# Optimization experiments

Hardware: AMD Instinct MI355X
Metric: run time of the kernel (lower is better)

## Reference

```python
import jax, jax.numpy as jnp
import numpy as np

N = 50000      # nodes
E = 1600000    # edges (avg degree 32)
F_IN = 128     # num_features
DIM = 64       # hidden dim
L = 3          # num_gc_layers
G = 500        # graphs in batch


def setup_inputs() -> dict:
    key = jax.random.key(0)
    ks = jax.random.split(key, 16)
    inp = {}
    inp["x"] = jax.random.normal(ks[0], (N, F_IN), dtype=jnp.float32)
    inp["edge_index"] = jax.random.randint(ks[1], (2, E), 0, N, dtype=jnp.int32)
    inp["batch"] = jnp.sort(jax.random.randint(ks[2], (N,), 0, G, dtype=jnp.int32))
    # GIN layer MLP params: layer0 maps F_IN->DIM->DIM, later layers DIM->DIM->DIM
    d_in = F_IN
    ki = 3
    for i in range(L):
        inp[f"W1_{i}"] = jax.random.normal(ks[ki], (d_in, DIM), dtype=jnp.float32) / np.sqrt(d_in); ki += 1
        inp[f"b1_{i}"] = jnp.zeros((DIM,), dtype=jnp.float32)
        inp[f"W2_{i}"] = jax.random.normal(ks[ki], (DIM, DIM), dtype=jnp.float32) / np.sqrt(DIM); ki += 1
        inp[f"b2_{i}"] = jnp.zeros((DIM,), dtype=jnp.float32)
        d_in = DIM
    # final scoring head: concat readout -> dim * L inputs, 1 output
    inp["Wm"] = jax.random.normal(ks[ki], (DIM * L, 1), dtype=jnp.float32) / np.sqrt(DIM * L)
    inp["bm"] = jnp.zeros((1,), dtype=jnp.float32)
    return inp


def _segment_softmax(scores, seg, num_segments):
    # numerically stable softmax over elements grouped by seg; scores [M, 1]
    m = jax.ops.segment_max(scores, seg, num_segments=num_segments)
    e = jnp.exp(scores - m[seg])
    denom = jax.ops.segment_sum(e, seg, num_segments=num_segments)
    return e / denom[seg]


def _forward(x, edge_index, batch, params):
    src, dst = edge_index[0], edge_index[1]
    n = x.shape[0]
    xs = []
    h = x
    for i in range(L):
        W1, b1, W2, b2 = params[4 * i: 4 * i + 4]
        # GINConv (eps=0): h_i <- MLP(h_i + sum_{j->i} h_j)
        agg = jax.ops.segment_sum(h[src], dst, num_segments=n)
        h = jax.nn.relu((h + agg) @ W1 + b1) @ W2 + b2
        if i != L - 1:
            h = jax.nn.relu(h)
        xs.append(h)
    node_prob = jnp.concatenate(xs, axis=1)            # concat readout [N, DIM*L]
    Wm, bm = params[4 * L], params[4 * L + 1]
    node_score = node_prob @ Wm + bm                   # [N, 1]
    # lift_node_score_to_edge_score
    src_score = node_score[src]                        # [E, 1]
    dst_score = node_score[dst]
    edge_score = src_score * dst_score
    edge_prop = _segment_softmax(edge_score, dst, n)   # softmax over edges per dst
    new_score = jax.ops.segment_sum(src_score * edge_prop, dst, num_segments=n)
    node_score = node_score + new_score
    # final softmax over nodes grouped by graph id
    return _segment_softmax(node_score, batch, G)


def reference(x, edge_index, batch, W1_0, b1_0, W2_0, b2_0, W1_1, b1_1, W2_1, b2_1,
              W1_2, b1_2, W2_2, b2_2, Wm, bm):
    params = [W1_0, b1_0, W2_0, b2_0, W1_1, b1_1, W2_1, b2_1,
              W1_2, b1_2, W2_2, b2_2, Wm, bm]
    return _forward(x, edge_index, batch, params)
```

## Files before the change

### kernel.cpp

```cpp
#include <hip/hip_runtime.h>
#include <math.h>

#define N_NODES 50000
#define N_EDGES 1600000
#define N_GRAPH 500
#define CHUNKS 64
#define EPC (N_EDGES / CHUNKS)

__device__ __forceinline__ float rl(float v, int k) {
    return __int_as_float(__builtin_amdgcn_readlane(__float_as_int(v), k));
}

__global__ __launch_bounds__(1024) void histsort_kernel(const int* __restrict__ src,
                                                        const int* __restrict__ dst,
                                                        int* __restrict__ csrc_chunk,
                                                        unsigned* __restrict__ cntloc,
                                                        unsigned short* __restrict__ lr_g) {
    __shared__ unsigned packed[N_NODES / 2];
    __shared__ unsigned aux[1024];
    const int c = blockIdx.x;
    const int s0 = c * EPC;
    const int tid = threadIdx.x;

    for (int i = tid; i < N_NODES / 2; i += 1024) packed[i] = 0;
    __syncthreads();

    for (int e = s0 + tid; e < s0 + EPC; e += 1024) {
        int d = dst[e];
        int sh = (d & 1) * 16;
        unsigned old = atomicAdd(&packed[d >> 1], 1u << sh);
        lr_g[e] = (unsigned short)((old >> sh) & 0xffffu);
    }
    __syncthreads();

    const int W = 25;
    int w0 = tid * W;
    int w1 = min(w0 + W, N_NODES / 2);
    unsigned run = 0;
    for (int i = w0; i < w1; i++) {
        unsigned v = packed[i];
        unsigned lo = v & 0xffffu, hi = v >> 16;
        packed[i] = run | ((run + lo) << 16);
        run += lo + hi;
    }
    aux[tid] = run;
    __syncthreads();
    for (int off = 1; off < 1024; off <<= 1) {
        unsigned t = (tid >= off) ? aux[tid - off] : 0;
        __syncthreads();
        aux[tid] += t;
        __syncthreads();
    }
    unsigned b0 = (tid == 0) ? 0 : aux[tid - 1];
    if (b0) {
        unsigned addv = b0 | (b0 << 16);
        for (int i = w0; i < w1; i++) packed[i] += addv;
    }
    __syncthreads();

    int* outc = csrc_chunk + (size_t)c * EPC;
    for (int e = s0 + tid; e < s0 + EPC; e += 1024) {
        int d = dst[e];
        unsigned pw = packed[d >> 1];
        unsigned loc = (d & 1) ? (pw >> 16) : (pw & 0xffffu);
        outc[loc + lr_g[e]] = src[e];
    }
    unsigned* clc = cntloc + (size_t)c * N_NODES;
    for (int d = tid; d < N_NODES; d += 1024) {
        unsigned pw = packed[d >> 1];
        unsigned loc = (d & 1) ? (pw >> 16) : (pw & 0xffffu);
        unsigned nxt;
        if (d + 1 < N_NODES) {
            unsigned pw2 = packed[(d + 1) >> 1];
            nxt = ((d + 1) & 1) ? (pw2 >> 16) : (pw2 & 0xffffu);
        } else {
            nxt = EPC;
        }
        clc[d] = ((nxt - loc) << 16) | loc;
    }
}

__global__ __launch_bounds__(1024) void base_scan1_kernel(const unsigned* __restrict__ cntloc,
                                                          unsigned short* __restrict__ base,
                                                          int* __restrict__ deg,
                                                          int* __restrict__ part, int N) {
    int d = blockIdx.x * 1024 + threadIdx.x;
    int run = 0;
    if (d < N) {
#pragma unroll 8
        for (int c = 0; c < CHUNKS; c++) {
            int v = (int)(cntloc[(size_t)c * N + d] >> 16);
            base[(size_t)c * N + d] = (unsigned short)run;
            run += v;
        }
        deg[d] = run;
    }
    int v = run;
#pragma unroll
    for (int o = 32; o >= 1; o >>= 1) v += __shfl_xor(v, o);
    __shared__ int red[16];
    if ((threadIdx.x & 63) == 0) red[threadIdx.x >> 6] = v;
    __syncthreads();
    if (threadIdx.x == 0) {
        int s = 0;
#pragma unroll
        for (int k = 0; k < 16; k++) s += red[k];
        part[blockIdx.x] = s;
    }
}

__global__ void scan2_kernel(int* __restrict__ part, int nb) {
    int lane = threadIdx.x;
    int v = (lane < nb) ? part[lane] : 0;
    int orig = v;
#pragma unroll
    for (int o = 1; o < 64; o <<= 1) {
        int t = __shfl_up(v, o);
        if (lane >= o) v += t;
    }
    if (lane < nb) part[lane] = v - orig;
    if (lane == nb - 1) part[nb] = v;
}

__global__ __launch_bounds__(1024) void scan3_kernel(const int* __restrict__ deg,
                                                     const int* __restrict__ part,
                                                     int* __restrict__ rowptr, int N) {
    int i = blockIdx.x * 1024 + threadIdx.x;
    int lane = threadIdx.x & 63;
    int w = threadIdx.x >> 6;
    int v = (i < N) ? deg[i] : 0;
    int inc = v;
#pragma unroll
    for (int o = 1; o < 64; o <<= 1) {
        int t = __shfl_up(inc, o);
        if (lane >= o) inc += t;
    }
    __shared__ int wsum[16];
    if (lane == 63) wsum[w] = inc;
    __syncthreads();
    if (threadIdx.x < 16) {
        int x = wsum[threadIdx.x];
        int xo = x;
#pragma unroll
        for (int o = 1; o < 16; o <<= 1) {
            int t = __shfl_up(x, o);
            if ((int)threadIdx.x >= o) x += t;
        }
        wsum[threadIdx.x] = x - xo;
    }
    __syncthreads();
    int b = part[blockIdx.x] + wsum[w];
    if (i < N) {
        rowptr[i] = b + inc - v;
        if (i == N - 1) rowptr[N] = b + inc;
    }
}

__global__ __launch_bounds__(256) void gatherfill_kernel(const int* __restrict__ csrc_chunk,
                                                         const unsigned* __restrict__ cntloc,
                                                         const unsigned short* __restrict__ base,
                                                         const int* __restrict__ rowptr,
                                                         int* __restrict__ csr_src) {
    const int perXcd = N_NODES / 8;
    int xcd = blockIdx.x & 7;
    int idx = (blockIdx.x >> 3) * 4 + ((threadIdx.x) >> 6);
    if (idx >= perXcd) return;
    int wid = xcd * perXcd + idx;
    int lane = threadIdx.x & 63;
    unsigned cl = cntloc[(size_t)lane * N_NODES + wid];
    int cnt = (int)(cl >> 16);
    int loc = (int)(cl & 0xffffu);
    int ob = rowptr[wid] + (int)base[(size_t)lane * N_NODES + wid];
    const int* in = csrc_chunk + (size_t)lane * EPC + loc;
    for (int i = 0; i < cnt; i++) csr_src[ob + i] = in[i];
}

__global__ __launch_bounds__(256) void agg_kernel(const float* __restrict__ y,
                                                  const int* __restrict__ rowptr,
                                                  const int* __restrict__ csr_src,
                                                  float* __restrict__ u, int N) {
    int wid = (blockIdx.x * 256 + threadIdx.x) >> 6;
    int lane = threadIdx.x & 63;
    if (wid >= N) return;
    int q = lane >> 4;
    int r = lane & 15;
    int start = rowptr[wid];
    int end = rowptr[wid + 1];
    float4 acc = make_float4(0.f, 0.f, 0.f, 0.f);
    int j = start;
    for (; j + 32 <= end; j += 32) {
        int s0 = csr_src[j + q];
        int s1 = csr_src[j + 4 + q];
        int s2 = csr_src[j + 8 + q];
        int s3 = csr_src[j + 12 + q];
        int s4 = csr_src[j + 16 + q];
        int s5 = csr_src[j + 20 + q];
        int s6 = csr_src[j + 24 + q];
        int s7 = csr_src[j + 28 + q];
        float4 v0 = *(const float4*)(y + (size_t)s0 * 64 + r * 4);
        float4 v1 = *(const float4*)(y + (size_t)s1 * 64 + r * 4);
        float4 v2 = *(const float4*)(y + (size_t)s2 * 64 + r * 4);
        float4 v3 = *(const float4*)(y + (size_t)s3 * 64 + r * 4);
        float4 v4 = *(const float4*)(y + (size_t)s4 * 64 + r * 4);
        float4 v5 = *(const float4*)(y + (size_t)s5 * 64 + r * 4);
        float4 v6 = *(const float4*)(y + (size_t)s6 * 64 + r * 4);
        float4 v7 = *(const float4*)(y + (size_t)s7 * 64 + r * 4);
        acc.x += ((v0.x + v1.x) + (v2.x + v3.x)) + ((v4.x + v5.x) + (v6.x + v7.x));
        acc.y += ((v0.y + v1.y) + (v2.y + v3.y)) + ((v4.y + v5.y) + (v6.y + v7.y));
        acc.z += ((v0.z + v1.z) + (v2.z + v3.z)) + ((v4.z + v5.z) + (v6.z + v7.z));
        acc.w += ((v0.w + v1.w) + (v2.w + v3.w)) + ((v4.w + v5.w) + (v6.w + v7.w));
    }
#pragma unroll
    for (int m = 0; m < 8; m++) {
        int e = j + 4 * m + q;
        if (e < end) {
            int s = csr_src[e];
            float4 v = *(const float4*)(y + (size_t)s * 64 + r * 4);
            acc.x += v.x; acc.y += v.y; acc.z += v.z; acc.w += v.w;
        }
    }
    acc.x += __shfl_xor(acc.x, 16);
    acc.y += __shfl_xor(acc.y, 16);
    acc.z += __shfl_xor(acc.z, 16);
    acc.w += __shfl_xor(acc.w, 16);
    acc.x += __shfl_xor(acc.x, 32);
    acc.y += __shfl_xor(acc.y, 32);
    acc.z += __shfl_xor(acc.z, 32);
    acc.w += __shfl_xor(acc.w, 32);
    if (lane < 16) {
        float4 self = *(const float4*)(y + (size_t)wid * 64 + r * 4);
        acc.x += self.x; acc.y += self.y; acc.z += self.z; acc.w += self.w;
        *(float4*)(u + (size_t)wid * 64 + r * 4) = acc;
    }
}

__global__ __launch_bounds__(256) void gemm0_kernel(const float* __restrict__ x,
                                                    const float* __restrict__ W1,
                                                    float* __restrict__ y0,
                                                    int N, int totalWaves) {
    int lane = threadIdx.x & 63;
    int wid = (blockIdx.x * 256 + threadIdx.x) >> 6;
    float w[64];
#pragma unroll
    for (int k = 0; k < 64; k++) w[k] = W1[k * 64 + lane];
    for (int node = wid; node < N; node += totalWaves) {
        float xa = x[node * 128 + lane];
        float a0 = 0.f, a1 = 0.f, a2 = 0.f, a3 = 0.f;
#pragma unroll
        for (int k = 0; k < 64; k += 4) {
            a0 = fmaf(rl(xa, k + 0), w[k + 0], a0);
            a1 = fmaf(rl(xa, k + 1), w[k + 1], a1);
            a2 = fmaf(rl(xa, k + 2), w[k + 2], a2);
            a3 = fmaf(rl(xa, k + 3), w[k + 3], a3);
        }
        y0[node * 64 + lane] = (a0 + a1) + (a2 + a3);
    }
#pragma unroll
    for (int k = 0; k < 64; k++) w[k] = W1[(64 + k) * 64 + lane];
    for (int node = wid; node < N; node += totalWaves) {
        float xb = x[node * 128 + 64 + lane];
        float a0 = 0.f, a1 = 0.f, a2 = 0.f, a3 = 0.f;
#pragma unroll
        for (int k = 0; k < 64; k += 4) {
            a0 = fmaf(rl(xb, k + 0), w[k + 0], a0);
            a1 = fmaf(rl(xb, k + 1), w[k + 1], a1);
            a2 = fmaf(rl(xb, k + 2), w[k + 2], a2);
            a3 = fmaf(rl(xb, k + 3), w[k + 3], a3);
        }
        y0[node * 64 + lane] += (a0 + a1) + (a2 + a3);
    }
}

template <int LAYER>
__global__ __launch_bounds__(256) void mlpAB_kernel(const float* __restrict__ u,
                                                    const float* __restrict__ b1,
                                                    const float* __restrict__ W2,
                                                    const float* __restrict__ b2,
                                                    const float* __restrict__ W1n,
                                                    const float* __restrict__ Wm,
                                                    float* __restrict__ ynext,
                                                    float* __restrict__ score,
                                                    int N, int totalWaves) {
    int lane = threadIdx.x & 63;
    int wid = (blockIdx.x * 256 + threadIdx.x) >> 6;
    float w2[64], w1[64];
#pragma unroll
    for (int k = 0; k < 64; k++) w2[k] = W2[k * 64 + lane];
#pragma unroll
    for (int k = 0; k < 64; k++) w1[k] = W1n[k * 64 + lane];
    float bb1 = b1[lane], bb2 = b2[lane], wm = Wm[LAYER * 64 + lane];

    int node = wid;
    float uin = (node < N) ? u[node * 64 + lane] : 0.f;
    for (; node < N; node += totalWaves) {
        int nn = node + totalWaves;
        float unext = (nn < N) ? u[nn * 64 + lane] : 0.f;
        float t = fmaxf(uin + bb1, 0.f);
        float a0 = 0.f, a1 = 0.f, a2 = 0.f, a3 = 0.f;
#pragma unroll
        for (int k = 0; k < 64; k += 4) {
            a0 = fmaf(rl(t, k + 0), w2[k + 0], a0);
            a1 = fmaf(rl(t, k + 1), w2[k + 1], a1);
            a2 = fmaf(rl(t, k + 2), w2[k + 2], a2);
            a3 = fmaf(rl(t, k + 3), w2[k + 3], a3);
        }
        float h = fmaxf(bb2 + ((a0 + a1) + (a2 + a3)), 0.f);
        float p = h * wm;
#pragma unroll
        for (int o = 32; o >= 1; o >>= 1) p += __shfl_xor(p, o);
        if (lane == 0) {
            if (LAYER == 0) score[node] = p;
            else score[node] += p;
        }
        float y0 = 0.f, y1 = 0.f, y2 = 0.f, y3 = 0.f;
#pragma unroll
        for (int k = 0; k < 64; k += 4) {
            y0 = fmaf(rl(h, k + 0), w1[k + 0], y0);
            y1 = fmaf(rl(h, k + 1), w1[k + 1], y1);
            y2 = fmaf(rl(h, k + 2), w1[k + 2], y2);
            y3 = fmaf(rl(h, k + 3), w1[k + 3], y3);
        }
        ynext[node * 64 + lane] = (y0 + y1) + (y2 + y3);
        uin = unext;
    }
}

__global__ __launch_bounds__(256) void mlpA2_kernel(const float* __restrict__ u,
                                                    const float* __restrict__ b1,
                                                    const float* __restrict__ W2,
                                                    const float* __restrict__ b2,
                                                    const float* __restrict__ Wm,
                                                    float* __restrict__ score,
                                                    int N, int totalWaves) {
    int lane = threadIdx.x & 63;
    int wid = (blockIdx.x * 256 + threadIdx.x) >> 6;
    float w2[64];
#pragma unroll
    for (int k = 0; k < 64; k++) w2[k] = W2[k * 64 + lane];
    float bb1 = b1[lane], bb2 = b2[lane], wm = Wm[2 * 64 + lane];

    int node = wid;
    float uin = (node < N) ? u[node * 64 + lane] : 0.f;
    for (; node < N; node += totalWaves) {
        int nn = node + totalWaves;
        float unext = (nn < N) ? u[nn * 64 + lane] : 0.f;
        float t = fmaxf(uin + bb1, 0.f);
        float a0 = 0.f, a1 = 0.f, a2 = 0.f, a3 = 0.f;
#pragma unroll
        for (int k = 0; k < 64; k += 4) {
            a0 = fmaf(rl(t, k + 0), w2[k + 0], a0);
            a1 = fmaf(rl(t, k + 1), w2[k + 1], a1);
            a2 = fmaf(rl(t, k + 2), w2[k + 2], a2);
            a3 = fmaf(rl(t, k + 3), w2[k + 3], a3);
        }
        float h = bb2 + ((a0 + a1) + (a2 + a3));
        float p = h * wm;
#pragma unroll
        for (int o = 32; o >= 1; o >>= 1) p += __shfl_xor(p, o);
        if (lane == 0) score[node] += p;
        uin = unext;
    }
}

__global__ __launch_bounds__(256) void edge_softmax_kernel(const float* __restrict__ score,
                                                           const int* __restrict__ rowptr,
                                                           const int* __restrict__ csr_src,
                                                           const float* __restrict__ bm,
                                                           float* __restrict__ nsf, int N) {
    int wid = (blockIdx.x * blockDim.x + threadIdx.x) >> 6;
    int lane = threadIdx.x & 63;
    if (wid >= N) return;
    float b = bm[0];
    float sd = score[wid] + b;
    int start = rowptr[wid];
    int end = rowptr[wid + 1];
    bool has0 = (start + lane < end);
    float ss0 = 0.f;
    float m = -INFINITY;
    if (has0) {
        ss0 = score[csr_src[start + lane]] + b;
        m = ss0 * sd;
    }
    for (int j = start + 64 + lane; j < end; j += 64) {
        float ss = score[csr_src[j]] + b;
        m = fmaxf(m, ss * sd);
    }
#pragma unroll
    for (int o = 32; o >= 1; o >>= 1) m = fmaxf(m, __shfl_xor(m, o));
    float se = 0.f, swe = 0.f;
    if (m > -INFINITY) {
        if (has0) {
            float e0 = expf(ss0 * sd - m);
            se += e0;
            swe += ss0 * e0;
        }
        for (int j = start + 64 + lane; j < end; j += 64) {
            float ss = score[csr_src[j]] + b;
            float e = expf(ss * sd - m);
            se += e;
            swe += ss * e;
        }
#pragma unroll
        for (int o = 32; o >= 1; o >>= 1) {
            se += __shfl_xor(se, o);
            swe += __shfl_xor(swe, o);
        }
    }
    float ns = (se > 0.f) ? (swe / se) : 0.f;
    if (lane == 0) nsf[wid] = sd + ns;
}

__global__ __launch_bounds__(256) void graph_softmax_kernel(const float* __restrict__ nsf,
                                                            const int* __restrict__ batch,
                                                            float* __restrict__ out, int N) {
    int g = blockIdx.x;
    int tid = threadIdx.x;
    int lo = 0, hi = N;
    while (lo < hi) { int mid = (lo + hi) >> 1; if (batch[mid] < g) lo = mid + 1; else hi = mid; }
    int s0 = lo;
    hi = N;
    while (lo < hi) { int mid = (lo + hi) >> 1; if (batch[mid] < g + 1) lo = mid + 1; else hi = mid; }
    int s1 = lo;

    __shared__ float red[4];
    __shared__ float bval;
    float m = -INFINITY;
    for (int i = s0 + tid; i < s1; i += 256) m = fmaxf(m, nsf[i]);
#pragma unroll
    for (int o = 32; o >= 1; o >>= 1) m = fmaxf(m, __shfl_xor(m, o));
    if ((tid & 63) == 0) red[tid >> 6] = m;
    __syncthreads();
    if (tid == 0) bval = fmaxf(fmaxf(red[0], red[1]), fmaxf(red[2], red[3]));
    __syncthreads();
    float bmx = bval;
    float s = 0.f;
    for (int i = s0 + tid; i < s1; i += 256) {
        float e = expf(nsf[i] - bmx);
        out[i] = e;
        s += e;
    }
#pragma unroll
    for (int o = 32; o >= 1; o >>= 1) s += __shfl_xor(s, o);
    __syncthreads();
    if ((tid & 63) == 0) red[tid >> 6] = s;
    __syncthreads();
    if (tid == 0) bval = red[0] + red[1] + red[2] + red[3];
    __syncthreads();
    float inv = 1.f / bval;
    for (int i = s0 + tid; i < s1; i += 256) out[i] *= inv;
}

extern "C" void kernel_launch(void* const* d_in, const int* in_sizes, int n_in,
                              void* d_out, int out_size, void* d_ws, size_t ws_size,
                              hipStream_t stream) {
    const int N = N_NODES, E = N_EDGES;

    const float* x = (const float*)d_in[0];
    const int* ei = (const int*)d_in[1];
    const int* batch = (const int*)d_in[2];
    const float* W1a[3] = {(const float*)d_in[3], (const float*)d_in[7], (const float*)d_in[11]};
    const float* b1a[3] = {(const float*)d_in[4], (const float*)d_in[8], (const float*)d_in[12]};
    const float* W2a[3] = {(const float*)d_in[5], (const float*)d_in[9], (const float*)d_in[13]};
    const float* b2a[3] = {(const float*)d_in[6], (const float*)d_in[10], (const float*)d_in[14]};
    const float* Wm = (const float*)d_in[15];
    const float* bm = (const float*)d_in[16];
    float* out = (float*)d_out;

    const int* srcp = ei;
    const int* dstp = ei + E;

    float* yA = (float*)d_ws;
    float* yB = yA + (size_t)N * 64;
    float* ubuf = yB + (size_t)N * 64;
    int* csrc_chunk = (int*)ubuf;
    float* score = ubuf + (size_t)N * 64;
    float* nsf = score + N;
    int* deg = (int*)(nsf + N);
    int* rowptr = deg + N;
    int* part = rowptr + N + 1;
    int* csr_src = part + 64;
    unsigned* cntloc = (unsigned*)(csr_src + E);
    unsigned short* base = (unsigned short*)(cntloc + (size_t)CHUNKS * N);
    unsigned short* lr = base + (size_t)CHUNKS * N;

    histsort_kernel<<<CHUNKS, 1024, 0, stream>>>(srcp, dstp, csrc_chunk, cntloc, lr);

    const int nbScan = (N + 1023) / 1024;
    base_scan1_kernel<<<nbScan, 1024, 0, stream>>>(cntloc, base, deg, part, N);
    scan2_kernel<<<1, 64, 0, stream>>>(part, nbScan);
    scan3_kernel<<<nbScan, 1024, 0, stream>>>(deg, part, rowptr, N);

    const int gfBlocks = 8 * ((N / 8 + 3) / 4);
    gatherfill_kernel<<<gfBlocks, 256, 0, stream>>>(csrc_chunk, cntloc, base, rowptr, csr_src);

    const int gw = 4096;
    gemm0_kernel<<<1024, 256, 0, stream>>>(x, W1a[0], yA, N, gw);

    int aggBlocks = (N + 3) / 4;

    agg_kernel<<<aggBlocks, 256, 0, stream>>>(yA, rowptr, csr_src, ubuf, N);
    mlpAB_kernel<0><<<1024, 256, 0, stream>>>(ubuf, b1a[0], W2a[0], b2a[0], W1a[1], Wm, yB, score, N, gw);

    agg_kernel<<<aggBlocks, 256, 0, stream>>>(yB, rowptr, csr_src, ubuf, N);
    mlpAB_kernel<1><<<1024, 256, 0, stream>>>(ubuf, b1a[1], W2a[1], b2a[1], W1a[2], Wm, yA, score, N, gw);

    agg_kernel<<<aggBlocks, 256, 0, stream>>>(yA, rowptr, csr_src, ubuf, N);
    mlpA2_kernel<<<1024, 256, 0, stream>>>(ubuf, b1a[2], W2a[2], b2a[2], Wm, score, N, gw);

    edge_softmax_kernel<<<(N + 3) / 4, 256, 0, stream>>>(score, rowptr, csr_src, bm, nsf, N);

    graph_softmax_kernel<<<N_GRAPH, 256, 0, stream>>>(nsf, batch, out, N);
}
```

Baseline: 374.1 us.

## Double histogram chunks, store compact per-chunk offsets, aggregate two nodes per wave

The CSR build now splits edges into 128 chunks instead of 64 and stores only 16-bit per-chunk start offsets (with a sentinel), deriving counts from adjacent offsets instead of storing packed count/offset words. The gather-fill kernel handles two chunks per lane. The aggregation kernel assigns two consecutive destination nodes to each wave and splits the accumulation by edge index, so short rows waste fewer idle lanes and fewer waves are launched. The trade-offs are per-edge branching in the accumulation, an extra shuffle reduction, and more scan work over the additional chunks.

```diff
diff --git a/kernel.cpp b/kernel.cpp
--- a/kernel.cpp
+++ b/kernel.cpp
@@ -4,8 +4,9 @@
 #define N_NODES 50000
 #define N_EDGES 1600000
 #define N_GRAPH 500
-#define CHUNKS 64
+#define CHUNKS 128
 #define EPC (N_EDGES / CHUNKS)
+#define NP1 (N_NODES + 1)
 
 __device__ __forceinline__ float rl(float v, int k) {
     return __int_as_float(__builtin_amdgcn_readlane(__float_as_int(v), k));
@@ -14,7 +15,7 @@
 __global__ __launch_bounds__(1024) void histsort_kernel(const int* __restrict__ src,
                                                         const int* __restrict__ dst,
                                                         int* __restrict__ csrc_chunk,
-                                                        unsigned* __restrict__ cntloc,
+                                                        unsigned short* __restrict__ locs,
                                                         unsigned short* __restrict__ lr_g) {
     __shared__ unsigned packed[N_NODES / 2];
     __shared__ unsigned aux[1024];
@@ -65,22 +66,20 @@
         unsigned loc = (d & 1) ? (pw >> 16) : (pw & 0xffffu);
         outc[loc + lr_g[e]] = src[e];
     }
-    unsigned* clc = cntloc + (size_t)c * N_NODES;
-    for (int d = tid; d < N_NODES; d += 1024) {
-        unsigned pw = packed[d >> 1];
-        unsigned loc = (d & 1) ? (pw >> 16) : (pw & 0xffffu);
-        unsigned nxt;
-        if (d + 1 < N_NODES) {
-            unsigned pw2 = packed[(d + 1) >> 1];
-            nxt = ((d + 1) & 1) ? (pw2 >> 16) : (pw2 & 0xffffu);
+    unsigned short* lc = locs + (size_t)c * NP1;
+    for (int d = tid; d <= N_NODES; d += 1024) {
+        unsigned short loc;
+        if (d == N_NODES) {
+            loc = (unsigned short)EPC;
         } else {
-            nxt = EPC;
-        }
-        clc[d] = ((nxt - loc) << 16) | loc;
-    }
-}
-
-__global__ __launch_bounds__(1024) void base_scan1_kernel(const unsigned* __restrict__ cntloc,
+            unsigned pw = packed[d >> 1];
+            loc = (unsigned short)((d & 1) ? (pw >> 16) : (pw & 0xffffu));
+        }
+        lc[d] = loc;
+    }
+}
+
+__global__ __launch_bounds__(1024) void base_scan1_kernel(const unsigned short* __restrict__ locs,
                                                           unsigned short* __restrict__ base,
                                                           int* __restrict__ deg,
                                                           int* __restrict__ part, int N) {
@@ -89,9 +88,10 @@
     if (d < N) {
 #pragma unroll 8
         for (int c = 0; c < CHUNKS; c++) {
-            int v = (int)(cntloc[(size_t)c * N + d] >> 16);
+            int l0 = locs[(size_t)c * NP1 + d];
+            int l1 = locs[(size_t)c * NP1 + d + 1];
             base[(size_t)c * N + d] = (unsigned short)run;
-            run += v;
+            run += l1 - l0;
         }
         deg[d] = run;
     }
@@ -157,46 +157,51 @@
 }
 
 __global__ __launch_bounds__(256) void gatherfill_kernel(const int* __restrict__ csrc_chunk,
-                                                         const unsigned* __restrict__ cntloc,
+                                                         const unsigned short* __restrict__ locs,
                                                          const unsigned short* __restrict__ base,
                                                          const int* __restrict__ rowptr,
                                                          int* __restrict__ csr_src) {
     const int perXcd = N_NODES / 8;
     int xcd = blockIdx.x & 7;
-    int idx = (blockIdx.x >> 3) * 4 + ((threadIdx.x) >> 6);
+    int idx = (blockIdx.x >> 3) * 4 + (threadIdx.x >> 6);
     if (idx >= perXcd) return;
     int wid = xcd * perXcd + idx;
     int lane = threadIdx.x & 63;
-    unsigned cl = cntloc[(size_t)lane * N_NODES + wid];
-    int cnt = (int)(cl >> 16);
-    int loc = (int)(cl & 0xffffu);
-    int ob = rowptr[wid] + (int)base[(size_t)lane * N_NODES + wid];
-    const int* in = csrc_chunk + (size_t)lane * EPC + loc;
-    for (int i = 0; i < cnt; i++) csr_src[ob + i] = in[i];
+    int rp = rowptr[wid];
+#pragma unroll
+    for (int cc = 0; cc < 2; cc++) {
+        int c = lane + cc * 64;
+        const unsigned short* lc = locs + (size_t)c * NP1;
+        int l0 = lc[wid];
+        int l1 = lc[wid + 1];
+        int cnt = l1 - l0;
+        int ob = rp + (int)base[(size_t)c * N_NODES + wid];
+        const int* in = csrc_chunk + (size_t)c * EPC + l0;
+        for (int i = 0; i < cnt; i++) csr_src[ob + i] = in[i];
+    }
 }
 
 __global__ __launch_bounds__(256) void agg_kernel(const float* __restrict__ y,
                                                   const int* __restrict__ rowptr,
                                                   const int* __restrict__ csr_src,
                                                   float* __restrict__ u, int N) {
-    int wid = (blockIdx.x * 256 + threadIdx.x) >> 6;
-    int lane = threadIdx.x & 63;
-    if (wid >= N) return;
+    int pair = (blockIdx.x * 256 + threadIdx.x) >> 6;
+    int n0 = pair * 2;
+    if (n0 >= N) return;
+    int lane = threadIdx.x & 63;
     int q = lane >> 4;
     int r = lane & 15;
-    int start = rowptr[wid];
-    int end = rowptr[wid + 1];
-    float4 acc = make_float4(0.f, 0.f, 0.f, 0.f);
-    int j = start;
-    for (; j + 32 <= end; j += 32) {
-        int s0 = csr_src[j + q];
-        int s1 = csr_src[j + 4 + q];
-        int s2 = csr_src[j + 8 + q];
-        int s3 = csr_src[j + 12 + q];
-        int s4 = csr_src[j + 16 + q];
-        int s5 = csr_src[j + 20 + q];
-        int s6 = csr_src[j + 24 + q];
-        int s7 = csr_src[j + 28 + q];
+    int s = rowptr[n0];
+    int b = rowptr[n0 + 1];
+    int e = rowptr[n0 + 2];
+    float4 A = make_float4(0.f, 0.f, 0.f, 0.f);
+    float4 B = make_float4(0.f, 0.f, 0.f, 0.f);
+    int j = s;
+    for (; j + 32 <= e; j += 32) {
+        int i0 = j + q,      i1 = j + 4 + q,  i2 = j + 8 + q,  i3 = j + 12 + q;
+        int i4 = j + 16 + q, i5 = j + 20 + q, i6 = j + 24 + q, i7 = j + 28 + q;
+        int s0 = csr_src[i0], s1 = csr_src[i1], s2 = csr_src[i2], s3 = csr_src[i3];
+        int s4 = csr_src[i4], s5 = csr_src[i5], s6 = csr_src[i6], s7 = csr_src[i7];
         float4 v0 = *(const float4*)(y + (size_t)s0 * 64 + r * 4);
         float4 v1 = *(const float4*)(y + (size_t)s1 * 64 + r * 4);
         float4 v2 = *(const float4*)(y + (size_t)s2 * 64 + r * 4);
@@ -205,32 +210,49 @@
         float4 v5 = *(const float4*)(y + (size_t)s5 * 64 + r * 4);
         float4 v6 = *(const float4*)(y + (size_t)s6 * 64 + r * 4);
         float4 v7 = *(const float4*)(y + (size_t)s7 * 64 + r * 4);
-        acc.x += ((v0.x + v1.x) + (v2.x + v3.x)) + ((v4.x + v5.x) + (v6.x + v7.x));
-        acc.y += ((v0.y + v1.y) + (v2.y + v3.y)) + ((v4.y + v5.y) + (v6.y + v7.y));
-        acc.z += ((v0.z + v1.z) + (v2.z + v3.z)) + ((v4.z + v5.z) + (v6.z + v7.z));
-        acc.w += ((v0.w + v1.w) + (v2.w + v3.w)) + ((v4.w + v5.w) + (v6.w + v7.w));
+        if (i0 < b) { A.x += v0.x; A.y += v0.y; A.z += v0.z; A.w += v0.w; }
+        else        { B.x += v0.x; B.y += v0.y; B.z += v0.z; B.w += v0.w; }
+        if (i1 < b) { A.x += v1.x; A.y += v1.y; A.z += v1.z; A.w += v1.w; }
+        else        { B.x += v1.x; B.y += v1.y; B.z += v1.z; B.w += v1.w; }
+        if (i2 < b) { A.x += v2.x; A.y += v2.y; A.z += v2.z; A.w += v2.w; }
+        else        { B.x += v2.x; B.y += v2.y; B.z += v2.z; B.w += v2.w; }
+        if (i3 < b) { A.x += v3.x; A.y += v3.y; A.z += v3.z; A.w += v3.w; }
+        else        { B.x += v3.x; B.y += v3.y; B.z += v3.z; B.w += v3.w; }
+        if (i4 < b) { A.x += v4.x; A.y += v4.y; A.z += v4.z; A.w += v4.w; }
+        else        { B.x += v4.x; B.y += v4.y; B.z += v4.z; B.w += v4.w; }
+        if (i5 < b) { A.x += v5.x; A.y += v5.y; A.z += v5.z; A.w += v5.w; }
+        else        { B.x += v5.x; B.y += v5.y; B.z += v5.z; B.w += v5.w; }
+        if (i6 < b) { A.x += v6.x; A.y += v6.y; A.z += v6.z; A.w += v6.w; }
+        else        { B.x += v6.x; B.y += v6.y; B.z += v6.z; B.w += v6.w; }
+        if (i7 < b) { A.x += v7.x; A.y += v7.y; A.z += v7.z; A.w += v7.w; }
+        else        { B.x += v7.x; B.y += v7.y; B.z += v7.z; B.w += v7.w; }
     }
 #pragma unroll
     for (int m = 0; m < 8; m++) {
-        int e = j + 4 * m + q;
-        if (e < end) {
-            int s = csr_src[e];
-            float4 v = *(const float4*)(y + (size_t)s * 64 + r * 4);
-            acc.x += v.x; acc.y += v.y; acc.z += v.z; acc.w += v.w;
-        }
-    }
-    acc.x += __shfl_xor(acc.x, 16);
-    acc.y += __shfl_xor(acc.y, 16);
-    acc.z += __shfl_xor(acc.z, 16);
-    acc.w += __shfl_xor(acc.w, 16);
-    acc.x += __shfl_xor(acc.x, 32);
-    acc.y += __shfl_xor(acc.y, 32);
-    acc.z += __shfl_xor(acc.z, 32);
-    acc.w += __shfl_xor(acc.w, 32);
+        int ii = j + 4 * m + q;
+        if (ii < e) {
+            int si = csr_src[ii];
+            float4 v = *(const float4*)(y + (size_t)si * 64 + r * 4);
+            if (ii < b) { A.x += v.x; A.y += v.y; A.z += v.z; A.w += v.w; }
+            else        { B.x += v.x; B.y += v.y; B.z += v.z; B.w += v.w; }
+        }
+    }
+    A.x += __shfl_xor(A.x, 16); A.y += __shfl_xor(A.y, 16);
+    A.z += __shfl_xor(A.z, 16); A.w += __shfl_xor(A.w, 16);
+    A.x += __shfl_xor(A.x, 32); A.y += __shfl_xor(A.y, 32);
+    A.z += __shfl_xor(A.z, 32); A.w += __shfl_xor(A.w, 32);
+    B.x += __shfl_xor(B.x, 16); B.y += __shfl_xor(B.y, 16);
+    B.z += __shfl_xor(B.z, 16); B.w += __shfl_xor(B.w, 16);
+    B.x += __shfl_xor(B.x, 32); B.y += __shfl_xor(B.y, 32);
+    B.z += __shfl_xor(B.z, 32); B.w += __shfl_xor(B.w, 32);
     if (lane < 16) {
-        float4 self = *(const float4*)(y + (size_t)wid * 64 + r * 4);
-        acc.x += self.x; acc.y += self.y; acc.z += self.z; acc.w += self.w;
-        *(float4*)(u + (size_t)wid * 64 + r * 4) = acc;
+        float4 self = *(const float4*)(y + (size_t)n0 * 64 + r * 4);
+        A.x += self.x; A.y += self.y; A.z += self.z; A.w += self.w;
+        *(float4*)(u + (size_t)n0 * 64 + r * 4) = A;
+    } else if (lane < 32) {
+        float4 self = *(const float4*)(y + (size_t)(n0 + 1) * 64 + r * 4);
+        B.x += self.x; B.y += self.y; B.z += self.z; B.w += self.w;
+        *(float4*)(u + (size_t)(n0 + 1) * 64 + r * 4) = B;
     }
 }
 
@@ -479,24 +501,24 @@
     int* rowptr = deg + N;
     int* part = rowptr + N + 1;
     int* csr_src = part + 64;
-    unsigned* cntloc = (unsigned*)(csr_src + E);
-    unsigned short* base = (unsigned short*)(cntloc + (size_t)CHUNKS * N);
+    unsigned short* locs = (unsigned short*)(csr_src + E);
+    unsigned short* base = locs + (size_t)CHUNKS * NP1;
     unsigned short* lr = base + (size_t)CHUNKS * N;
 
-    histsort_kernel<<<CHUNKS, 1024, 0, stream>>>(srcp, dstp, csrc_chunk, cntloc, lr);
+    histsort_kernel<<<CHUNKS, 1024, 0, stream>>>(srcp, dstp, csrc_chunk, locs, lr);
 
     const int nbScan = (N + 1023) / 1024;
-    base_scan1_kernel<<<nbScan, 1024, 0, stream>>>(cntloc, base, deg, part, N);
+    base_scan1_kernel<<<nbScan, 1024, 0, stream>>>(locs, base, deg, part, N);
     scan2_kernel<<<1, 64, 0, stream>>>(part, nbScan);
     scan3_kernel<<<nbScan, 1024, 0, stream>>>(deg, part, rowptr, N);
 
     const int gfBlocks = 8 * ((N / 8 + 3) / 4);
-    gatherfill_kernel<<<gfBlocks, 256, 0, stream>>>(csrc_chunk, cntloc, base, rowptr, csr_src);
+    gatherfill_kernel<<<gfBlocks, 256, 0, stream>>>(csrc_chunk, locs, base, rowptr, csr_src);
 
     const int gw = 4096;
     gemm0_kernel<<<1024, 256, 0, stream>>>(x, W1a[0], yA, N, gw);
 
-    int aggBlocks = (N + 3) / 4;
+    int aggBlocks = (N / 2 + 3) / 4;
 
     agg_kernel<<<aggBlocks, 256, 0, stream>>>(yA, rowptr, csr_src, ubuf, N);
     mlpAB_kernel<0><<<1024, 256, 0, stream>>>(ubuf, b1a[0], W2a[0], b2a[0], W1a[1], Wm, yB, score, N, gw);
```

New measurement: 383.7 us. 1.03x slower.
